# Kernel optimization log

Measured on AMD Instinct MI355X. Metric: run time of the kernel, lower is better.

Reference implementation:

```python
import jax, jax.numpy as jnp
import numpy as np

HEADS = 8
CH = 256
DH = CH // HEADS  # 32
NB = 128          # nb_features
EPS = 1e-4


def setup_inputs() -> dict:
    key = jax.random.key(0)
    ks = jax.random.split(key, 8)
    b, c, h, w = 4, CH, 96, 96
    s = 1.0 / np.sqrt(CH)  # typical linear init scale
    x = jax.random.normal(ks[0], (b, c, h, w), dtype=jnp.float32)
    wq = jax.random.normal(ks[1], (CH, CH), dtype=jnp.float32) * s
    wk = jax.random.normal(ks[2], (CH, CH), dtype=jnp.float32) * s
    wv = jax.random.normal(ks[3], (CH, CH), dtype=jnp.float32) * s
    wo = jax.random.normal(ks[4], (CH, CH), dtype=jnp.float32) * s
    bo = jnp.zeros((CH,), dtype=jnp.float32)
    # FAVOR+ gaussian orthogonal random projection (nb_features, dim_head)
    pm = np.random.default_rng(0)
    blocks = []
    for _ in range(NB // DH):
        qmat, _ = np.linalg.qr(pm.standard_normal((DH, DH)))
        blocks.append(qmat.T)
    proj = np.concatenate(blocks, axis=0)
    # scale rows to chi-distributed norms (scaling=0 default in performer_pytorch)
    norms = np.linalg.norm(pm.standard_normal((NB, DH)), axis=1, keepdims=True)
    proj_mat = jnp.asarray(proj * norms, dtype=jnp.float32)
    wp = jax.random.normal(ks[5], (CH, CH, 1, 1), dtype=jnp.float32) * s
    bp = jnp.zeros((CH,), dtype=jnp.float32)
    return {"x": x, "wq": wq, "wk": wk, "wv": wv, "wo": wo, "bo": bo,
            "proj_mat": proj_mat, "wp": wp, "bp": bp}


def softmax_kernel(data, proj, is_query):
    # data: (b, h, n, d); proj: (m, d). Performer FAVOR+ positive softmax features.
    data_normalizer = data.shape[-1] ** -0.25
    ratio = proj.shape[0] ** -0.5
    data_dash = jnp.einsum('bhnd,md->bhnm', data * data_normalizer, proj)
    diag = (jnp.sum(data * data, axis=-1) * 0.5 * (data_normalizer ** 2))[..., None]
    if is_query:
        m = jnp.max(data_dash, axis=-1, keepdims=True)
    else:
        m = jnp.max(data_dash, axis=(-1, -2), keepdims=True)
    return ratio * (jnp.exp(data_dash - diag - m) + EPS)


def reference(x, wq, wk, wv, wo, bo, proj_mat, wp, bp):
    b, c, h, w = x.shape
    n = h * w
    xf = x.reshape(b, c, n).transpose(0, 2, 1)  # (b, n, c)

    def split_heads(t):
        return t.reshape(b, n, HEADS, DH).transpose(0, 2, 1, 3)  # (b, h, n, d)

    q = split_heads(xf @ wq.T)
    k = split_heads(xf @ wk.T)
    v = split_heads(xf @ wv.T)

    qp = softmax_kernel(q, proj_mat, True)   # (b, h, n, m)
    kp = softmax_kernel(k, proj_mat, False)  # (b, h, n, m)

    # non-causal linear attention
    k_sum = jnp.sum(kp, axis=-2)                                   # (b, h, m)
    d_inv = 1.0 / jnp.einsum('bhnm,bhm->bhn', qp, k_sum)           # (b, h, n)
    ctx = jnp.einsum('bhnm,bhnd->bhmd', kp, v)                     # (b, h, m, d)
    out = jnp.einsum('bhnm,bhmd->bhnd', qp, ctx) * d_inv[..., None]

    out = out.transpose(0, 2, 1, 3).reshape(b, n, c)  # merge heads
    out = out @ wo.T + bo                              # to_out (attn_out_bias=True)
    out = out.transpose(0, 2, 1).reshape(b, c, h, w)
    # 1x1 conv projection
    out = jnp.einsum('bchw,oc->bohw', out, wp[:, :, 0, 0]) + bp[None, :, None, None]
    return out
```

## Files before the change

kernel.cpp:

```cpp
#include <hip/hip_runtime.h>

#define NTOT 9216
#define NORMC 0.42044820762685725f
#define RATIO 0.08838834764831845f
#define FEPS 1e-4f

typedef _Float16 h8 __attribute__((ext_vector_type(8)));
typedef _Float16 h4 __attribute__((ext_vector_type(4)));
typedef float f4 __attribute__((ext_vector_type(4)));

__device__ __forceinline__ void gld16(const _Float16* g, _Float16* l) {
  __builtin_amdgcn_global_load_lds((const __attribute__((address_space(1))) void*)g,
                                   (__attribute__((address_space(3))) void*)l, 16, 0, 0);
}

__global__ __launch_bounds__(256) void prep(
    const float* __restrict__ x, const float* __restrict__ wq,
    const float* __restrict__ wk, const float* __restrict__ wv,
    const float* __restrict__ proj, const float* __restrict__ wo,
    const float* __restrict__ bo, const float* __restrict__ wp,
    const float* __restrict__ bp, _Float16* __restrict__ xT,
    _Float16* __restrict__ Wall, _Float16* __restrict__ projh,
    _Float16* __restrict__ Wc, float* __restrict__ bc) {
  __shared__ float T_s[64][65];
  int r = blockIdx.x, t = threadIdx.x;
  if (r < 2304) {
    int nx = r % 144, rem = r / 144;
    int cy = rem & 3, b = rem >> 2;
    int n0 = nx * 64, c0 = cy * 64;
    for (int i = 0; i < 4; ++i) {
      int f = t + i * 256;
      int cc = f >> 4, n4 = f & 15;
      float4 a = *(const float4*)(x + ((size_t)(b * 256 + c0 + cc)) * NTOT + n0 + n4 * 4);
      T_s[cc][n4 * 4 + 0] = a.x;
      T_s[cc][n4 * 4 + 1] = a.y;
      T_s[cc][n4 * 4 + 2] = a.z;
      T_s[cc][n4 * 4 + 3] = a.w;
    }
    __syncthreads();
    for (int i = 0; i < 2; ++i) {
      int f = t + i * 256;
      int nn = f >> 3, c8 = f & 7;
      h8 hv;
      for (int j = 0; j < 8; ++j) hv[j] = (_Float16)T_s[c8 * 8 + j][nn];
      *(h8*)(xT + ((size_t)(b * NTOT + n0 + nn)) * 256 + c0 + c8 * 8) = hv;
    }
    return;
  }
  int r2 = r - 2304;
  if (r2 < 768) {
    const float* src = (r2 < 256) ? wq + (size_t)r2 * 256
                     : (r2 < 512) ? wk + (size_t)(r2 - 256) * 256
                                  : wv + (size_t)(r2 - 512) * 256;
    Wall[(size_t)r2 * 256 + t] = (_Float16)src[t];
  } else if (r2 < 784) {
    int idx = (r2 - 768) * 256 + t;
    projh[idx] = (_Float16)proj[idx];
  } else {
    int o = r2 - 784;
    float acc = 0.f;
    for (int c = 0; c < 256; ++c) acc += wp[o * 256 + c] * wo[c * 256 + t];
    Wc[o * 256 + t] = (_Float16)acc;
    if (t == 0) {
      float ab = bp[o];
      for (int c = 0; c < 256; ++c) ab += wp[o * 256 + c] * bo[c];
      bc[o] = ab;
    }
  }
}

__global__ __launch_bounds__(256) void qkv_mfma(
    const _Float16* __restrict__ xT, const _Float16* __restrict__ Wall,
    const _Float16* __restrict__ projh, _Float16* __restrict__ q,
    _Float16* __restrict__ k, _Float16* __restrict__ vT,
    float* __restrict__ kmaxp) {
  __shared__ __align__(16) _Float16 A_s[128 * 32];
  __shared__ __align__(16) _Float16 B_s[128 * 32];
  __shared__ __align__(16) _Float16 ktile[64 * 132];
  int bx = blockIdx.x, co0 = blockIdx.y * 128, sel = blockIdx.z;
  int b = bx / 72, ntile = bx % 72;
  int n0 = bx * 128;
  const _Float16* Wb = Wall + (size_t)sel * 65536;
  int t = threadIdx.x, wave = t >> 6, lane = t & 63;
  int lm = lane & 15, lg = lane >> 4;
  int wm = (wave & 1) * 64, wn = (wave >> 1) * 64;
  int srow = wave * 32 + (lane >> 2);
  int scol = ((lane & 3) ^ ((lane >> 3) & 3)) * 8;
  const _Float16* gA = Wb + (size_t)(co0 + srow) * 256 + scol;
  const _Float16* gB = xT + (size_t)(n0 + srow) * 256 + scol;
  _Float16* lA = A_s + wave * 1024;
  _Float16* lB = B_s + wave * 1024;
  int pg = (lg ^ ((lm >> 1) & 3)) * 8;
  f4 acc[4][4] = {};
  if (sel < 2) {
    for (int kt = 0; kt < 8; ++kt) {
      int c0 = kt * 32;
      __syncthreads();
      gld16(gA + c0, lA);
      gld16(gA + c0 + 16 * 256, lA + 512);
      gld16(gB + c0, lB);
      gld16(gB + c0 + 16 * 256, lB + 512);
      __syncthreads();
      h8 a[4], bf[4];
#pragma unroll
      for (int mi = 0; mi < 4; ++mi) a[mi] = *(const h8*)&A_s[(wm + mi * 16 + lm) * 32 + pg];
#pragma unroll
      for (int ni = 0; ni < 4; ++ni) bf[ni] = *(const h8*)&B_s[(wn + ni * 16 + lm) * 32 + pg];
#pragma unroll
      for (int mi = 0; mi < 4; ++mi)
#pragma unroll
        for (int ni = 0; ni < 4; ++ni)
          acc[mi][ni] = __builtin_amdgcn_mfma_f32_16x16x32_f16(a[mi], bf[ni], acc[mi][ni], 0, 0, 0);
    }
    _Float16* Out = (sel == 0) ? q : k;
#pragma unroll
    for (int mi = 0; mi < 4; ++mi)
#pragma unroll
      for (int ni = 0; ni < 4; ++ni) {
        h4 hv;
#pragma unroll
        for (int r = 0; r < 4; ++r) hv[r] = (_Float16)acc[mi][ni][r];
        *(h4*)(Out + (size_t)(n0 + wn + ni * 16 + lm) * 256 + co0 + wm + mi * 16 + lg * 4) = hv;
      }
    if (sel == 1) {
      h8 pr[8];
#pragma unroll
      for (int mt = 0; mt < 8; ++mt)
        pr[mt] = *(const h8*)&projh[(mt * 16 + lm) * 32 + lg * 8];
      float vmax = -1e30f;
      for (int half = 0; half < 2; ++half) {
        __syncthreads();
        if ((wave >> 1) == half) {
#pragma unroll
          for (int mi = 0; mi < 4; ++mi)
#pragma unroll
            for (int ni = 0; ni < 4; ++ni) {
              h4 hv;
#pragma unroll
              for (int r = 0; r < 4; ++r) hv[r] = (_Float16)acc[mi][ni][r];
              *(h4*)&ktile[(ni * 16 + lm) * 132 + wm + mi * 16 + lg * 4] = hv;
            }
        }
        __syncthreads();
#pragma unroll
        for (int nt2 = 0; nt2 < 4; ++nt2) {
          h8 a = *(const h8*)&ktile[(nt2 * 16 + lm) * 132 + wave * 32 + lg * 8];
#pragma unroll
          for (int mt = 0; mt < 8; ++mt) {
            f4 z = {0.f, 0.f, 0.f, 0.f};
            f4 d = __builtin_amdgcn_mfma_f32_16x16x32_f16(a, pr[mt], z, 0, 0, 0);
            vmax = fmaxf(vmax, fmaxf(fmaxf(d[0], d[1]), fmaxf(d[2], d[3])));
          }
        }
      }
      for (int i = 1; i < 64; i <<= 1) vmax = fmaxf(vmax, __shfl_xor(vmax, i, 64));
      if (lane == 0) {
        int h = (co0 >> 5) + wave;
        kmaxp[(size_t)(b * 8 + h) * 72 + ntile] = NORMC * vmax;
      }
    }
  } else {
    for (int kt = 0; kt < 8; ++kt) {
      int c0 = kt * 32;
      __syncthreads();
      gld16(gA + c0, lA);
      gld16(gA + c0 + 16 * 256, lA + 512);
      gld16(gB + c0, lB);
      gld16(gB + c0 + 16 * 256, lB + 512);
      __syncthreads();
      h8 a[4], bf[4];
#pragma unroll
      for (int mi = 0; mi < 4; ++mi) a[mi] = *(const h8*)&A_s[(wm + mi * 16 + lm) * 32 + pg];
#pragma unroll
      for (int ni = 0; ni < 4; ++ni) bf[ni] = *(const h8*)&B_s[(wn + ni * 16 + lm) * 32 + pg];
#pragma unroll
      for (int mi = 0; mi < 4; ++mi)
#pragma unroll
        for (int ni = 0; ni < 4; ++ni)
          acc[mi][ni] = __builtin_amdgcn_mfma_f32_16x16x32_f16(bf[ni], a[mi], acc[mi][ni], 0, 0, 0);
    }
#pragma unroll
    for (int mi = 0; mi < 4; ++mi)
#pragma unroll
      for (int ni = 0; ni < 4; ++ni) {
        h4 hv;
#pragma unroll
        for (int r = 0; r < 4; ++r) hv[r] = (_Float16)acc[mi][ni][r];
        *(h4*)(vT + ((size_t)(b * 256 + co0 + wm + mi * 16 + lm)) * NTOT +
               ntile * 128 + wn + ni * 16 + lg * 4) = hv;
      }
  }
}

__global__ __launch_bounds__(256) void ctx_mfma(
    const _Float16* __restrict__ k, const _Float16* __restrict__ vT,
    const _Float16* __restrict__ projh, const float* __restrict__ kmaxp,
    float* __restrict__ part) {
  __shared__ __align__(16) _Float16 k_s[128 * 32];
  __shared__ __align__(16) _Float16 vT_s[32 * 136];
  __shared__ __align__(16) _Float16 kpT[128 * 136];
  __shared__ float diag_s[128];
  __shared__ float kmax_sh;
  int bh = blockIdx.y, b = bh >> 3, h = bh & 7;
  int nbase = blockIdx.x * 384;
  int t = threadIdx.x, wave = t >> 6, lane = t & 63, lm = lane & 15, lg = lane >> 4;
  h8 pr[8];
#pragma unroll
  for (int mt = 0; mt < 8; ++mt) pr[mt] = *(const h8*)&projh[(mt * 16 + lm) * 32 + lg * 8];
  {
    float* kred = (float*)kpT;
    if (t < 72) kred[t] = kmaxp[(size_t)bh * 72 + t];
    __syncthreads();
    if (t == 0) {
      float mx = -1e30f;
      for (int i = 0; i < 72; ++i) mx = fmaxf(mx, kred[i]);
      kmax_sh = mx;
    }
    __syncthreads();
  }
  float kmax = kmax_sh;
  int scol = ((lane & 3) ^ ((lane >> 3) & 3)) * 8;
  const _Float16* gK =
      k + ((size_t)(b * NTOT + nbase + wave * 32 + (lane >> 2))) * 256 + h * 32 + scol;
  const _Float16* gV = vT + ((size_t)(b * 256 + h * 32 + (t >> 3))) * NTOT + nbase;
  _Float16* lK = k_s + wave * 1024;
  int pg = (lg ^ ((lm >> 1) & 3)) * 8;
  f4 cacc[2][2] = {};
  float ks[8] = {};
  for (int ch = 0; ch < 3; ++ch) {
    gld16(gK + (size_t)(ch * 128) * 256, lK);
    gld16(gK + (size_t)(ch * 128) * 256 + 16 * 256, lK + 512);
    {
      int d = t >> 3, g = t & 7;
#pragma unroll
      for (int i = 0; i < 2; ++i)
        *(h8*)&vT_s[d * 136 + (i * 8 + g) * 8] = *(const h8*)(gV + ch * 128 + (i * 8 + g) * 8);
    }
    __syncthreads();
    if (t < 128) {
      float s = 0.f;
#pragma unroll
      for (int c = 0; c < 4; ++c) {
        h8 kv = *(const h8*)&k_s[t * 32 + c * 8];
#pragma unroll
        for (int j = 0; j < 8; ++j) s += (float)kv[j] * (float)kv[j];
      }
      diag_s[t] = s * (0.5f * NORMC * NORMC);
    }
    f4 dsh[2][8];
#pragma unroll
    for (int nt = 0; nt < 2; ++nt) {
      h8 a = *(const h8*)&k_s[(wave * 32 + nt * 16 + lm) * 32 + pg];
#pragma unroll
      for (int mt = 0; mt < 8; ++mt) {
        f4 z = {0.f, 0.f, 0.f, 0.f};
        dsh[nt][mt] = __builtin_amdgcn_mfma_f32_16x16x32_f16(a, pr[mt], z, 0, 0, 0);
      }
    }
    __syncthreads();
#pragma unroll
    for (int nt = 0; nt < 2; ++nt)
#pragma unroll
      for (int mt = 0; mt < 8; ++mt) {
        h4 hv;
        float lsum = 0.f;
#pragma unroll
        for (int r = 0; r < 4; ++r) {
          int nl = wave * 32 + nt * 16 + lg * 4 + r;
          float val = RATIO * (__expf(NORMC * dsh[nt][mt][r] - diag_s[nl] - kmax) + FEPS);
          hv[r] = (_Float16)val;
          lsum += val;
        }
        ks[mt] += lsum;
        *(h4*)&kpT[(mt * 16 + lm) * 136 + wave * 32 + nt * 16 + lg * 4] = hv;
      }
    __syncthreads();
#pragma unroll
    for (int k2 = 0; k2 < 4; ++k2) {
      h8 a2[2], b2[2];
#pragma unroll
      for (int mt2 = 0; mt2 < 2; ++mt2)
        a2[mt2] = *(const h8*)&kpT[(wave * 32 + mt2 * 16 + lm) * 136 + k2 * 32 + lg * 8];
#pragma unroll
      for (int dt = 0; dt < 2; ++dt)
        b2[dt] = *(const h8*)&vT_s[(dt * 16 + lm) * 136 + k2 * 32 + lg * 8];
#pragma unroll
      for (int mt2 = 0; mt2 < 2; ++mt2)
#pragma unroll
        for (int dt = 0; dt < 2; ++dt)
          cacc[mt2][dt] =
              __builtin_amdgcn_mfma_f32_16x16x32_f16(a2[mt2], b2[dt], cacc[mt2][dt], 0, 0, 0);
    }
    __syncthreads();
  }
  float* pp = part + (size_t)(blockIdx.y * 24 + blockIdx.x) * 4224;
#pragma unroll
  for (int mt2 = 0; mt2 < 2; ++mt2)
#pragma unroll
    for (int dt = 0; dt < 2; ++dt)
      *(f4*)(pp + (dt * 16 + lm) * 128 + wave * 32 + mt2 * 16 + lg * 4) = cacc[mt2][dt];
  float* redk = (float*)kpT;
#pragma unroll
  for (int mt = 0; mt < 8; ++mt) {
    float s = ks[mt];
    s += __shfl_xor(s, 16, 64);
    s += __shfl_xor(s, 32, 64);
    if (lg == 0) redk[wave * 128 + mt * 16 + lm] = s;
  }
  __syncthreads();
  if (t < 128)
    pp[32 * 128 + t] = redk[t] + redk[128 + t] + redk[256 + t] + redk[384 + t];
}

__global__ __launch_bounds__(256) void reduce_ctx(
    const float* __restrict__ part, _Float16* __restrict__ ctxT_g,
    float* __restrict__ ksum_g) {
  int bh = blockIdx.x >> 2, qtr = blockIdx.x & 3;
  int t = threadIdx.x;
  const float* pb = part + (size_t)bh * 24 * 4224;
  for (int it = 0; it < 5; ++it) {
    int lc = it * 256 + t;
    if (lc < 1056) {
      int cell = qtr * 1056 + lc;
      float s = 0.f;
      for (int p = 0; p < 24; ++p) s += pb[(size_t)p * 4224 + cell];
      int d = cell >> 7, m = cell & 127;
      if (d < 32) ctxT_g[(size_t)bh * 4096 + d * 128 + m] = (_Float16)s;
      else ksum_g[(size_t)bh * 128 + m] = s;
    }
  }
}

__global__ __launch_bounds__(256) void attn_mfma(
    const _Float16* __restrict__ q, const _Float16* __restrict__ projh,
    const _Float16* __restrict__ ctxT_g, const float* __restrict__ ksum_g,
    _Float16* __restrict__ attn) {
  __shared__ __align__(16) _Float16 q_sh[128 * 32];
  __shared__ __align__(16) _Float16 qp_s[128 * 136];
  __shared__ float ksum_s[128];
  int n0 = blockIdx.x * 128;
  int bh = blockIdx.y, b = bh >> 3, h = bh & 7;
  int t = threadIdx.x, wave = t >> 6, lane = t & 63, lm = lane & 15, lg = lane >> 4;
  h8 pr[8];
#pragma unroll
  for (int mt = 0; mt < 8; ++mt) pr[mt] = *(const h8*)&projh[(mt * 16 + lm) * 32 + lg * 8];
  int scol = ((lane & 3) ^ ((lane >> 3) & 3)) * 8;
  const _Float16* gQ =
      q + ((size_t)(b * NTOT + n0 + wave * 32 + (lane >> 2))) * 256 + h * 32 + scol;
  gld16(gQ, q_sh + wave * 1024);
  gld16(gQ + 16 * 256, q_sh + wave * 1024 + 512);
  h8 ac[2][4];
#pragma unroll
  for (int dt = 0; dt < 2; ++dt)
#pragma unroll
    for (int k2 = 0; k2 < 4; ++k2)
      ac[dt][k2] = *(const h8*)&ctxT_g[(size_t)bh * 4096 + (dt * 16 + lm) * 128 + k2 * 32 + lg * 8];
  if (t < 128) ksum_s[t] = ksum_g[(size_t)bh * 128 + t];
  __syncthreads();
  int pg = (lg ^ ((lm >> 1) & 3)) * 8;
  float diag_r[2];
#pragma unroll
  for (int nt = 0; nt < 2; ++nt) {
    int n = wave * 32 + nt * 16 + lm;
    float s = 0.f;
#pragma unroll
    for (int c = 0; c < 4; ++c) {
      h8 qv = *(const h8*)&q_sh[n * 32 + c * 8];
#pragma unroll
      for (int j = 0; j < 8; ++j) s += (float)qv[j] * (float)qv[j];
    }
    diag_r[nt] = s * (0.5f * NORMC * NORMC);
  }
  f4 dsh[2][8];
#pragma unroll
  for (int nt = 0; nt < 2; ++nt) {
    h8 qf = *(const h8*)&q_sh[(wave * 32 + nt * 16 + lm) * 32 + pg];
#pragma unroll
    for (int mt = 0; mt < 8; ++mt) {
      f4 z = {0.f, 0.f, 0.f, 0.f};
      dsh[nt][mt] = __builtin_amdgcn_mfma_f32_16x16x32_f16(pr[mt], qf, z, 0, 0, 0);
    }
  }
  float den_r[2];
#pragma unroll
  for (int nt = 0; nt < 2; ++nt) {
    float mx = -1e30f;
#pragma unroll
    for (int mt = 0; mt < 8; ++mt)
#pragma unroll
      for (int r = 0; r < 4; ++r) mx = fmaxf(mx, dsh[nt][mt][r]);
    mx = fmaxf(mx, __shfl_xor(mx, 16, 64));
    mx = fmaxf(mx, __shfl_xor(mx, 32, 64));
    float den = 0.f;
#pragma unroll
    for (int mt = 0; mt < 8; ++mt) {
      h4 hv;
#pragma unroll
      for (int r = 0; r < 4; ++r) {
        float val = RATIO * (__expf(NORMC * (dsh[nt][mt][r] - mx) - diag_r[nt]) + FEPS);
        hv[r] = (_Float16)val;
        den += val * ksum_s[mt * 16 + lg * 4 + r];
      }
      *(h4*)&qp_s[(wave * 32 + nt * 16 + lm) * 136 + mt * 16 + lg * 4] = hv;
    }
    den += __shfl_xor(den, 16, 64);
    den += __shfl_xor(den, 32, 64);
    den_r[nt] = 1.f / den;
  }
  __syncthreads();
  f4 oacc[2][2] = {};
#pragma unroll
  for (int k2 = 0; k2 < 4; ++k2) {
    h8 bq[2];
#pragma unroll
    for (int nt = 0; nt < 2; ++nt)
      bq[nt] = *(const h8*)&qp_s[(wave * 32 + nt * 16 + lm) * 136 + k2 * 32 + lg * 8];
#pragma unroll
    for (int dt = 0; dt < 2; ++dt)
#pragma unroll
      for (int nt = 0; nt < 2; ++nt)
        oacc[dt][nt] = __builtin_amdgcn_mfma_f32_16x16x32_f16(ac[dt][k2], bq[nt], oacc[dt][nt], 0, 0, 0);
  }
#pragma unroll
  for (int dt = 0; dt < 2; ++dt)
#pragma unroll
    for (int nt = 0; nt < 2; ++nt) {
      int n = wave * 32 + nt * 16 + lm;
      h4 hv;
#pragma unroll
      for (int r = 0; r < 4; ++r) hv[r] = (_Float16)(oacc[dt][nt][r] * den_r[nt]);
      *(h4*)(attn + ((size_t)(b * NTOT + n0 + n)) * 256 + h * 32 + dt * 16 + lg * 4) = hv;
    }
}

__global__ __launch_bounds__(256) void out_mfma(
    const _Float16* __restrict__ Wc, const _Float16* __restrict__ attn,
    const float* __restrict__ bc, float* __restrict__ out) {
  __shared__ __align__(16) _Float16 A_s[128 * 32];
  __shared__ __align__(16) _Float16 B_s[128 * 32];
  int bx = blockIdx.x;
  int o0 = blockIdx.y * 128;
  int b = bx / 72, nb0 = (bx % 72) * 128;
  int t = threadIdx.x, wave = t >> 6, lane = t & 63;
  int lm = lane & 15, lg = lane >> 4;
  int wm = (wave & 1) * 64, wn = (wave >> 1) * 64;
  int srow = wave * 32 + (lane >> 2);
  int scol = ((lane & 3) ^ ((lane >> 3) & 3)) * 8;
  const _Float16* gA = Wc + (size_t)(o0 + srow) * 256 + scol;
  const _Float16* gB = attn + (size_t)(b * NTOT + nb0 + srow) * 256 + scol;
  _Float16* lA = A_s + wave * 1024;
  _Float16* lB = B_s + wave * 1024;
  int pg = (lg ^ ((lm >> 1) & 3)) * 8;
  f4 acc[4][4] = {};
  for (int kt = 0; kt < 8; ++kt) {
    int c0 = kt * 32;
    __syncthreads();
    gld16(gA + c0, lA);
    gld16(gA + c0 + 16 * 256, lA + 512);
    gld16(gB + c0, lB);
    gld16(gB + c0 + 16 * 256, lB + 512);
    __syncthreads();
    h8 a[4], bf[4];
#pragma unroll
    for (int mi = 0; mi < 4; ++mi) a[mi] = *(const h8*)&A_s[(wm + mi * 16 + lm) * 32 + pg];
#pragma unroll
    for (int ni = 0; ni < 4; ++ni) bf[ni] = *(const h8*)&B_s[(wn + ni * 16 + lm) * 32 + pg];
#pragma unroll
    for (int mi = 0; mi < 4; ++mi)
#pragma unroll
      for (int ni = 0; ni < 4; ++ni)
        acc[mi][ni] = __builtin_amdgcn_mfma_f32_16x16x32_f16(bf[ni], a[mi], acc[mi][ni], 0, 0, 0);
  }
#pragma unroll
  for (int mi = 0; mi < 4; ++mi) {
    int o = o0 + wm + mi * 16 + lm;
    float bias = bc[o];
#pragma unroll
    for (int ni = 0; ni < 4; ++ni) {
      f4 ov = acc[mi][ni];
      float4 st = make_float4(ov[0] + bias, ov[1] + bias, ov[2] + bias, ov[3] + bias);
      *(float4*)(out + ((size_t)(b * 256 + o)) * NTOT + nb0 + wn + ni * 16 + lg * 4) = st;
    }
  }
}

extern "C" void kernel_launch(void* const* d_in, const int* in_sizes, int n_in,
                              void* d_out, int out_size, void* d_ws, size_t ws_size,
                              hipStream_t stream) {
  const float* x = (const float*)d_in[0];
  const float* wq = (const float*)d_in[1];
  const float* wk = (const float*)d_in[2];
  const float* wv = (const float*)d_in[3];
  const float* wo = (const float*)d_in[4];
  const float* bo = (const float*)d_in[5];
  const float* proj = (const float*)d_in[6];
  const float* wp = (const float*)d_in[7];
  const float* bp = (const float*)d_in[8];
  float* out = (float*)d_out;
  float* ws = (float*)d_ws;

  float* part = ws;
  float* kmaxp = part + 3244032;
  float* ksum_g = kmaxp + 2304;
  float* bc = ksum_g + 4096;
  _Float16* hb = (_Float16*)(bc + 256);
  const size_t THALF = (size_t)4 * NTOT * 256;
  _Float16* q_h = hb;
  _Float16* k_h = q_h + THALF;
  _Float16* xT = k_h + THALF;
  _Float16* vTg = xT + THALF;
  _Float16* Wall = vTg + THALF;
  _Float16* Wc = Wall + 768 * 256;
  _Float16* projh = Wc + 65536;
  _Float16* ctxT_g = projh + 4096;

  prep<<<3344, 256, 0, stream>>>(x, wq, wk, wv, proj, wo, bo, wp, bp,
                                 xT, Wall, projh, Wc, bc);
  qkv_mfma<<<dim3(288, 2, 3), 256, 0, stream>>>(xT, Wall, projh, q_h, k_h, vTg, kmaxp);
  ctx_mfma<<<dim3(24, 32), 256, 0, stream>>>(k_h, vTg, projh, kmaxp, part);
  reduce_ctx<<<128, 256, 0, stream>>>(part, ctxT_g, ksum_g);
  attn_mfma<<<dim3(72, 32), 256, 0, stream>>>(q_h, projh, ctxT_g, ksum_g, xT);
  out_mfma<<<dim3(288, 2), 256, 0, stream>>>(Wc, xT, bc, out);
}
```

Before: 216.6 us.

## Double-buffer LDS tiles in GEMM kernels and prefetch K chunks in ctx

The qkv and out GEMM kernels now keep two LDS stages in a shared pool. The next K-slice's global-to-LDS loads are issued before the MFMAs on the current slice, and each iteration has one barrier instead of two. The two separate q/k and v loop copies in qkv are merged into one loop with a select on MFMA operand order. In ctx_mfma the first K tile load is issued before the kmax reduction, and later tiles are prefetched after the barrier, so load latency overlaps with compute. LDS use grows in the GEMMs (32KB, with ktile aliased onto the pool), which may lower occupancy. The correctness of async-load ordering depends on the single barrier per iteration.

```diff
diff --git a/kernel.cpp b/kernel.cpp
--- a/kernel.cpp
+++ b/kernel.cpp
@@ -74,9 +74,7 @@
     const _Float16* __restrict__ projh, _Float16* __restrict__ q,
     _Float16* __restrict__ k, _Float16* __restrict__ vT,
     float* __restrict__ kmaxp) {
-  __shared__ __align__(16) _Float16 A_s[128 * 32];
-  __shared__ __align__(16) _Float16 B_s[128 * 32];
-  __shared__ __align__(16) _Float16 ktile[64 * 132];
+  __shared__ __align__(16) _Float16 pool[16384];
   int bx = blockIdx.x, co0 = blockIdx.y * 128, sel = blockIdx.z;
   int b = bx / 72, ntile = bx % 72;
   int n0 = bx * 128;
@@ -88,30 +86,48 @@
   int scol = ((lane & 3) ^ ((lane >> 3) & 3)) * 8;
   const _Float16* gA = Wb + (size_t)(co0 + srow) * 256 + scol;
   const _Float16* gB = xT + (size_t)(n0 + srow) * 256 + scol;
-  _Float16* lA = A_s + wave * 1024;
-  _Float16* lB = B_s + wave * 1024;
+  int so = wave * 1024;
   int pg = (lg ^ ((lm >> 1) & 3)) * 8;
   f4 acc[4][4] = {};
-  if (sel < 2) {
-    for (int kt = 0; kt < 8; ++kt) {
-      int c0 = kt * 32;
-      __syncthreads();
-      gld16(gA + c0, lA);
-      gld16(gA + c0 + 16 * 256, lA + 512);
-      gld16(gB + c0, lB);
-      gld16(gB + c0 + 16 * 256, lB + 512);
-      __syncthreads();
-      h8 a[4], bf[4];
-#pragma unroll
-      for (int mi = 0; mi < 4; ++mi) a[mi] = *(const h8*)&A_s[(wm + mi * 16 + lm) * 32 + pg];
-#pragma unroll
-      for (int ni = 0; ni < 4; ++ni) bf[ni] = *(const h8*)&B_s[(wn + ni * 16 + lm) * 32 + pg];
+  gld16(gA, pool + so);
+  gld16(gA + 16 * 256, pool + so + 512);
+  gld16(gB, pool + 8192 + so);
+  gld16(gB + 16 * 256, pool + 8192 + so + 512);
+  __syncthreads();
+#pragma unroll
+  for (int kt = 0; kt < 8; ++kt) {
+    int cur = (kt & 1) << 12;
+    int nxt = cur ^ 4096;
+    if (kt < 7) {
+      int c0 = (kt + 1) * 32;
+      gld16(gA + c0, pool + nxt + so);
+      gld16(gA + c0 + 16 * 256, pool + nxt + so + 512);
+      gld16(gB + c0, pool + 8192 + nxt + so);
+      gld16(gB + c0 + 16 * 256, pool + 8192 + nxt + so + 512);
+    }
+    h8 a[4], bf[4];
+#pragma unroll
+    for (int mi = 0; mi < 4; ++mi)
+      a[mi] = *(const h8*)&pool[cur + (wm + mi * 16 + lm) * 32 + pg];
+#pragma unroll
+    for (int ni = 0; ni < 4; ++ni)
+      bf[ni] = *(const h8*)&pool[8192 + cur + (wn + ni * 16 + lm) * 32 + pg];
+    if (sel < 2) {
 #pragma unroll
       for (int mi = 0; mi < 4; ++mi)
 #pragma unroll
         for (int ni = 0; ni < 4; ++ni)
           acc[mi][ni] = __builtin_amdgcn_mfma_f32_16x16x32_f16(a[mi], bf[ni], acc[mi][ni], 0, 0, 0);
-    }
+    } else {
+#pragma unroll
+      for (int mi = 0; mi < 4; ++mi)
+#pragma unroll
+        for (int ni = 0; ni < 4; ++ni)
+          acc[mi][ni] = __builtin_amdgcn_mfma_f32_16x16x32_f16(bf[ni], a[mi], acc[mi][ni], 0, 0, 0);
+    }
+    __syncthreads();
+  }
+  if (sel < 2) {
     _Float16* Out = (sel == 0) ? q : k;
 #pragma unroll
     for (int mi = 0; mi < 4; ++mi)
@@ -123,6 +139,7 @@
         *(h4*)(Out + (size_t)(n0 + wn + ni * 16 + lm) * 256 + co0 + wm + mi * 16 + lg * 4) = hv;
       }
     if (sel == 1) {
+      _Float16* ktile = pool;
       h8 pr[8];
 #pragma unroll
       for (int mt = 0; mt < 8; ++mt)
@@ -160,25 +177,6 @@
       }
     }
   } else {
-    for (int kt = 0; kt < 8; ++kt) {
-      int c0 = kt * 32;
-      __syncthreads();
-      gld16(gA + c0, lA);
-      gld16(gA + c0 + 16 * 256, lA + 512);
-      gld16(gB + c0, lB);
-      gld16(gB + c0 + 16 * 256, lB + 512);
-      __syncthreads();
-      h8 a[4], bf[4];
-#pragma unroll
-      for (int mi = 0; mi < 4; ++mi) a[mi] = *(const h8*)&A_s[(wm + mi * 16 + lm) * 32 + pg];
-#pragma unroll
-      for (int ni = 0; ni < 4; ++ni) bf[ni] = *(const h8*)&B_s[(wn + ni * 16 + lm) * 32 + pg];
-#pragma unroll
-      for (int mi = 0; mi < 4; ++mi)
-#pragma unroll
-        for (int ni = 0; ni < 4; ++ni)
-          acc[mi][ni] = __builtin_amdgcn_mfma_f32_16x16x32_f16(bf[ni], a[mi], acc[mi][ni], 0, 0, 0);
-    }
 #pragma unroll
     for (int mi = 0; mi < 4; ++mi)
 #pragma unroll
@@ -207,29 +205,29 @@
   h8 pr[8];
 #pragma unroll
   for (int mt = 0; mt < 8; ++mt) pr[mt] = *(const h8*)&projh[(mt * 16 + lm) * 32 + lg * 8];
-  {
-    float* kred = (float*)kpT;
-    if (t < 72) kred[t] = kmaxp[(size_t)bh * 72 + t];
-    __syncthreads();
-    if (t == 0) {
-      float mx = -1e30f;
-      for (int i = 0; i < 72; ++i) mx = fmaxf(mx, kred[i]);
-      kmax_sh = mx;
-    }
-    __syncthreads();
-  }
-  float kmax = kmax_sh;
   int scol = ((lane & 3) ^ ((lane >> 3) & 3)) * 8;
   const _Float16* gK =
       k + ((size_t)(b * NTOT + nbase + wave * 32 + (lane >> 2))) * 256 + h * 32 + scol;
   const _Float16* gV = vT + ((size_t)(b * 256 + h * 32 + (t >> 3))) * NTOT + nbase;
   _Float16* lK = k_s + wave * 1024;
+  gld16(gK, lK);
+  gld16(gK + 16 * 256, lK + 512);
+  {
+    float* kred = (float*)kpT;
+    if (t < 72) kred[t] = kmaxp[(size_t)bh * 72 + t];
+    __syncthreads();
+    if (t == 0) {
+      float mx = -1e30f;
+      for (int i = 0; i < 72; ++i) mx = fmaxf(mx, kred[i]);
+      kmax_sh = mx;
+    }
+    __syncthreads();
+  }
+  float kmax = kmax_sh;
   int pg = (lg ^ ((lm >> 1) & 3)) * 8;
   f4 cacc[2][2] = {};
   float ks[8] = {};
   for (int ch = 0; ch < 3; ++ch) {
-    gld16(gK + (size_t)(ch * 128) * 256, lK);
-    gld16(gK + (size_t)(ch * 128) * 256 + 16 * 256, lK + 512);
     {
       int d = t >> 3, g = t & 7;
 #pragma unroll
@@ -258,6 +256,10 @@
       }
     }
     __syncthreads();
+    if (ch < 2) {
+      gld16(gK + (size_t)((ch + 1) * 128) * 256, lK);
+      gld16(gK + (size_t)((ch + 1) * 128) * 256 + 16 * 256, lK + 512);
+    }
 #pragma unroll
     for (int nt = 0; nt < 2; ++nt)
 #pragma unroll
@@ -436,8 +438,7 @@
 __global__ __launch_bounds__(256) void out_mfma(
     const _Float16* __restrict__ Wc, const _Float16* __restrict__ attn,
     const float* __restrict__ bc, float* __restrict__ out) {
-  __shared__ __align__(16) _Float16 A_s[128 * 32];
-  __shared__ __align__(16) _Float16 B_s[128 * 32];
+  __shared__ __align__(16) _Float16 pool[16384];
   int bx = blockIdx.x;
   int o0 = blockIdx.y * 128;
   int b = bx / 72, nb0 = (bx % 72) * 128;
@@ -448,28 +449,38 @@
   int scol = ((lane & 3) ^ ((lane >> 3) & 3)) * 8;
   const _Float16* gA = Wc + (size_t)(o0 + srow) * 256 + scol;
   const _Float16* gB = attn + (size_t)(b * NTOT + nb0 + srow) * 256 + scol;
-  _Float16* lA = A_s + wave * 1024;
-  _Float16* lB = B_s + wave * 1024;
+  int so = wave * 1024;
   int pg = (lg ^ ((lm >> 1) & 3)) * 8;
   f4 acc[4][4] = {};
+  gld16(gA, pool + so);
+  gld16(gA + 16 * 256, pool + so + 512);
+  gld16(gB, pool + 8192 + so);
+  gld16(gB + 16 * 256, pool + 8192 + so + 512);
+  __syncthreads();
+#pragma unroll
   for (int kt = 0; kt < 8; ++kt) {
-    int c0 = kt * 32;
-    __syncthreads();
-    gld16(gA + c0, lA);
-    gld16(gA + c0 + 16 * 256, lA + 512);
-    gld16(gB + c0, lB);
-    gld16(gB + c0 + 16 * 256, lB + 512);
-    __syncthreads();
+    int cur = (kt & 1) << 12;
+    int nxt = cur ^ 4096;
+    if (kt < 7) {
+      int c0 = (kt + 1) * 32;
+      gld16(gA + c0, pool + nxt + so);
+      gld16(gA + c0 + 16 * 256, pool + nxt + so + 512);
+      gld16(gB + c0, pool + 8192 + nxt + so);
+      gld16(gB + c0 + 16 * 256, pool + 8192 + nxt + so + 512);
+    }
     h8 a[4], bf[4];
 #pragma unroll
-    for (int mi = 0; mi < 4; ++mi) a[mi] = *(const h8*)&A_s[(wm + mi * 16 + lm) * 32 + pg];
-#pragma unroll
-    for (int ni = 0; ni < 4; ++ni) bf[ni] = *(const h8*)&B_s[(wn + ni * 16 + lm) * 32 + pg];
+    for (int mi = 0; mi < 4; ++mi)
+      a[mi] = *(const h8*)&pool[cur + (wm + mi * 16 + lm) * 32 + pg];
+#pragma unroll
+    for (int ni = 0; ni < 4; ++ni)
+      bf[ni] = *(const h8*)&pool[8192 + cur + (wn + ni * 16 + lm) * 32 + pg];
 #pragma unroll
     for (int mi = 0; mi < 4; ++mi)
 #pragma unroll
       for (int ni = 0; ni < 4; ++ni)
         acc[mi][ni] = __builtin_amdgcn_mfma_f32_16x16x32_f16(bf[ni], a[mi], acc[mi][ni], 0, 0, 0);
+    __syncthreads();
   }
 #pragma unroll
   for (int mi = 0; mi < 4; ++mi) {
```

After: 219.7 us. No clear change (+1.5%).

## Remap blocks to XCDs for L2 locality and software-pipeline ctx/out loads

Applied to the files above, without the earlier changes.

Flattens the grids of qkv, ctx, attn and out kernels and remaps block IDs so that blocks sharing the same input tile or (batch, head) land on the same XCD, improving L2 reuse. ctx_mfma prefetches the next chunk of K (via global_load_lds) and V (into registers) during the current chunk's compute. out_mfma uses double-buffered LDS with partial vmcnt waits in place of full syncthreads. These changes add manual waitcnt and barrier handling, which risks ordering bugs, and the double buffer uses more LDS.

```diff
diff --git a/kernel.cpp b/kernel.cpp
--- a/kernel.cpp
+++ b/kernel.cpp
@@ -77,7 +77,12 @@
   __shared__ __align__(16) _Float16 A_s[128 * 32];
   __shared__ __align__(16) _Float16 B_s[128 * 32];
   __shared__ __align__(16) _Float16 ktile[64 * 132];
-  int bx = blockIdx.x, co0 = blockIdx.y * 128, sel = blockIdx.z;
+  int id = blockIdx.x;
+  int xcd = id & 7, slot = id >> 3;
+  int bx = xcd * 36 + slot / 6;
+  int variant = slot % 6;
+  int sel = variant % 3;
+  int co0 = (variant / 3) * 128;
   int b = bx / 72, ntile = bx % 72;
   int n0 = bx * 128;
   const _Float16* Wb = Wall + (size_t)sel * 65536;
@@ -201,12 +206,27 @@
   __shared__ __align__(16) _Float16 kpT[128 * 136];
   __shared__ float diag_s[128];
   __shared__ float kmax_sh;
-  int bh = blockIdx.y, b = bh >> 3, h = bh & 7;
-  int nbase = blockIdx.x * 384;
+  int id = blockIdx.x;
+  int xcd = id & 7, slot = id >> 3;
+  int grp = xcd * 12 + slot / 8;
+  int h = slot % 8;
+  int nx = grp % 24, b = grp / 24;
+  int bh = b * 8 + h;
+  int nbase = nx * 384;
   int t = threadIdx.x, wave = t >> 6, lane = t & 63, lm = lane & 15, lg = lane >> 4;
   h8 pr[8];
 #pragma unroll
   for (int mt = 0; mt < 8; ++mt) pr[mt] = *(const h8*)&projh[(mt * 16 + lm) * 32 + lg * 8];
+  int scol = ((lane & 3) ^ ((lane >> 3) & 3)) * 8;
+  const _Float16* gK =
+      k + ((size_t)(b * NTOT + nbase + wave * 32 + (lane >> 2))) * 256 + h * 32 + scol;
+  const _Float16* gV = vT + ((size_t)(b * 256 + h * 32 + (t >> 3))) * NTOT + nbase;
+  _Float16* lK = k_s + wave * 1024;
+  int vd = t >> 3, vg = t & 7;
+  gld16(gK, lK);
+  gld16(gK + 16 * 256, lK + 512);
+  h8 vr0 = *(const h8*)(gV + vg * 8);
+  h8 vr1 = *(const h8*)(gV + 64 + vg * 8);
   {
     float* kred = (float*)kpT;
     if (t < 72) kred[t] = kmaxp[(size_t)bh * 72 + t];
@@ -219,24 +239,16 @@
     __syncthreads();
   }
   float kmax = kmax_sh;
-  int scol = ((lane & 3) ^ ((lane >> 3) & 3)) * 8;
-  const _Float16* gK =
-      k + ((size_t)(b * NTOT + nbase + wave * 32 + (lane >> 2))) * 256 + h * 32 + scol;
-  const _Float16* gV = vT + ((size_t)(b * 256 + h * 32 + (t >> 3))) * NTOT + nbase;
-  _Float16* lK = k_s + wave * 1024;
   int pg = (lg ^ ((lm >> 1) & 3)) * 8;
   f4 cacc[2][2] = {};
   float ks[8] = {};
+#pragma unroll 1
   for (int ch = 0; ch < 3; ++ch) {
-    gld16(gK + (size_t)(ch * 128) * 256, lK);
-    gld16(gK + (size_t)(ch * 128) * 256 + 16 * 256, lK + 512);
-    {
-      int d = t >> 3, g = t & 7;
-#pragma unroll
-      for (int i = 0; i < 2; ++i)
-        *(h8*)&vT_s[d * 136 + (i * 8 + g) * 8] = *(const h8*)(gV + ch * 128 + (i * 8 + g) * 8);
-    }
-    __syncthreads();
+    *(h8*)&vT_s[vd * 136 + vg * 8] = vr0;
+    *(h8*)&vT_s[vd * 136 + 64 + vg * 8] = vr1;
+    asm volatile("s_waitcnt vmcnt(0) lgkmcnt(0)" ::: "memory");
+    __builtin_amdgcn_s_barrier();
+    __builtin_amdgcn_sched_barrier(0);
     if (t < 128) {
       float s = 0.f;
 #pragma unroll
@@ -257,7 +269,15 @@
         dsh[nt][mt] = __builtin_amdgcn_mfma_f32_16x16x32_f16(a, pr[mt], z, 0, 0, 0);
       }
     }
-    __syncthreads();
+    asm volatile("s_waitcnt lgkmcnt(0)" ::: "memory");
+    __builtin_amdgcn_s_barrier();
+    __builtin_amdgcn_sched_barrier(0);
+    if (ch < 2) {
+      gld16(gK + (size_t)((ch + 1) * 128) * 256, lK);
+      gld16(gK + (size_t)((ch + 1) * 128) * 256 + 16 * 256, lK + 512);
+      vr0 = *(const h8*)(gV + (ch + 1) * 128 + vg * 8);
+      vr1 = *(const h8*)(gV + (ch + 1) * 128 + 64 + vg * 8);
+    }
 #pragma unroll
     for (int nt = 0; nt < 2; ++nt)
 #pragma unroll
@@ -274,7 +294,9 @@
         ks[mt] += lsum;
         *(h4*)&kpT[(mt * 16 + lm) * 136 + wave * 32 + nt * 16 + lg * 4] = hv;
       }
-    __syncthreads();
+    asm volatile("s_waitcnt lgkmcnt(0)" ::: "memory");
+    __builtin_amdgcn_s_barrier();
+    __builtin_amdgcn_sched_barrier(0);
 #pragma unroll
     for (int k2 = 0; k2 < 4; ++k2) {
       h8 a2[2], b2[2];
@@ -291,9 +313,9 @@
           cacc[mt2][dt] =
               __builtin_amdgcn_mfma_f32_16x16x32_f16(a2[mt2], b2[dt], cacc[mt2][dt], 0, 0, 0);
     }
-    __syncthreads();
-  }
-  float* pp = part + (size_t)(blockIdx.y * 24 + blockIdx.x) * 4224;
+    __builtin_amdgcn_s_barrier();
+  }
+  float* pp = part + (size_t)(bh * 24 + nx) * 4224;
 #pragma unroll
   for (int mt2 = 0; mt2 < 2; ++mt2)
 #pragma unroll
@@ -338,8 +360,13 @@
   __shared__ __align__(16) _Float16 q_sh[128 * 32];
   __shared__ __align__(16) _Float16 qp_s[128 * 136];
   __shared__ float ksum_s[128];
-  int n0 = blockIdx.x * 128;
-  int bh = blockIdx.y, b = bh >> 3, h = bh & 7;
+  int id = blockIdx.x;
+  int xcd = id & 7, slot = id >> 3;
+  int grp = xcd * 36 + slot / 8;
+  int h = slot % 8;
+  int nb = grp % 72, b = grp / 72;
+  int bh = b * 8 + h;
+  int n0 = nb * 128;
   int t = threadIdx.x, wave = t >> 6, lane = t & 63, lm = lane & 15, lg = lane >> 4;
   h8 pr[8];
 #pragma unroll
@@ -436,11 +463,12 @@
 __global__ __launch_bounds__(256) void out_mfma(
     const _Float16* __restrict__ Wc, const _Float16* __restrict__ attn,
     const float* __restrict__ bc, float* __restrict__ out) {
-  __shared__ __align__(16) _Float16 A_s[128 * 32];
-  __shared__ __align__(16) _Float16 B_s[128 * 32];
-  int bx = blockIdx.x;
-  int o0 = blockIdx.y * 128;
-  int b = bx / 72, nb0 = (bx % 72) * 128;
+  __shared__ __align__(16) _Float16 pool[16384];
+  int id = blockIdx.x;
+  int xcd = id & 7, slot = id >> 3;
+  int tile = xcd * 36 + slot / 2;
+  int o0 = (slot & 1) * 128;
+  int b = tile / 72, nb0 = (tile % 72) * 128;
   int t = threadIdx.x, wave = t >> 6, lane = t & 63;
   int lm = lane & 15, lg = lane >> 4;
   int wm = (wave & 1) * 64, wn = (wave >> 1) * 64;
@@ -448,28 +476,42 @@
   int scol = ((lane & 3) ^ ((lane >> 3) & 3)) * 8;
   const _Float16* gA = Wc + (size_t)(o0 + srow) * 256 + scol;
   const _Float16* gB = attn + (size_t)(b * NTOT + nb0 + srow) * 256 + scol;
-  _Float16* lA = A_s + wave * 1024;
-  _Float16* lB = B_s + wave * 1024;
+  int so = wave * 1024;
   int pg = (lg ^ ((lm >> 1) & 3)) * 8;
   f4 acc[4][4] = {};
+  gld16(gA, pool + so);
+  gld16(gA + 16 * 256, pool + so + 512);
+  gld16(gB, pool + 8192 + so);
+  gld16(gB + 16 * 256, pool + 8192 + so + 512);
+#pragma unroll 1
   for (int kt = 0; kt < 8; ++kt) {
-    int c0 = kt * 32;
-    __syncthreads();
-    gld16(gA + c0, lA);
-    gld16(gA + c0 + 16 * 256, lA + 512);
-    gld16(gB + c0, lB);
-    gld16(gB + c0 + 16 * 256, lB + 512);
-    __syncthreads();
+    int cur = (kt & 1) << 12;
+    int nxt = cur ^ 4096;
+    if (kt < 7) {
+      int c0 = (kt + 1) * 32;
+      gld16(gA + c0, pool + nxt + so);
+      gld16(gA + c0 + 16 * 256, pool + nxt + so + 512);
+      gld16(gB + c0, pool + 8192 + nxt + so);
+      gld16(gB + c0 + 16 * 256, pool + 8192 + nxt + so + 512);
+      asm volatile("s_waitcnt vmcnt(4)" ::: "memory");
+    } else {
+      asm volatile("s_waitcnt vmcnt(0)" ::: "memory");
+    }
+    __builtin_amdgcn_s_barrier();
+    __builtin_amdgcn_sched_barrier(0);
     h8 a[4], bf[4];
 #pragma unroll
-    for (int mi = 0; mi < 4; ++mi) a[mi] = *(const h8*)&A_s[(wm + mi * 16 + lm) * 32 + pg];
-#pragma unroll
-    for (int ni = 0; ni < 4; ++ni) bf[ni] = *(const h8*)&B_s[(wn + ni * 16 + lm) * 32 + pg];
+    for (int mi = 0; mi < 4; ++mi)
+      a[mi] = *(const h8*)&pool[cur + (wm + mi * 16 + lm) * 32 + pg];
+#pragma unroll
+    for (int ni = 0; ni < 4; ++ni)
+      bf[ni] = *(const h8*)&pool[8192 + cur + (wn + ni * 16 + lm) * 32 + pg];
 #pragma unroll
     for (int mi = 0; mi < 4; ++mi)
 #pragma unroll
       for (int ni = 0; ni < 4; ++ni)
         acc[mi][ni] = __builtin_amdgcn_mfma_f32_16x16x32_f16(bf[ni], a[mi], acc[mi][ni], 0, 0, 0);
+    __builtin_amdgcn_s_barrier();
   }
 #pragma unroll
   for (int mi = 0; mi < 4; ++mi) {
@@ -516,9 +558,9 @@
 
   prep<<<3344, 256, 0, stream>>>(x, wq, wk, wv, proj, wo, bo, wp, bp,
                                  xT, Wall, projh, Wc, bc);
-  qkv_mfma<<<dim3(288, 2, 3), 256, 0, stream>>>(xT, Wall, projh, q_h, k_h, vTg, kmaxp);
-  ctx_mfma<<<dim3(24, 32), 256, 0, stream>>>(k_h, vTg, projh, kmaxp, part);
+  qkv_mfma<<<1728, 256, 0, stream>>>(xT, Wall, projh, q_h, k_h, vTg, kmaxp);
+  ctx_mfma<<<768, 256, 0, stream>>>(k_h, vTg, projh, kmaxp, part);
   reduce_ctx<<<128, 256, 0, stream>>>(part, ctxT_g, ksum_g);
-  attn_mfma<<<dim3(72, 32), 256, 0, stream>>>(q_h, projh, ctxT_g, ksum_g, xT);
-  out_mfma<<<dim3(288, 2), 256, 0, stream>>>(Wc, xT, bc, out);
-}
+  attn_mfma<<<2304, 256, 0, stream>>>(q_h, projh, ctxT_g, ksum_g, xT);
+  out_mfma<<<576, 256, 0, stream>>>(Wc, xT, bc, out);
+}
```

After: 220.3 us. Within noise of the previous version (+1.7%).

## Prefetch next K/V chunk in ctx kernel, alias shared buffers, widen reduce grid

Applied to the files above, without the earlier changes.

In ctx_mfma the next chunk's K tile (async global-to-LDS) and V rows (into registers) are now loaded while the exp/feature stage runs, and syncthreads are replaced with explicit waitcnt plus s_barrier. This hides global load latency behind compute. qkv_mfma and attn_mfma alias their shared buffers into one pool to cut LDS use and raise occupancy, which needs an added barrier in attn_mfma. reduce_ctx is reshaped into 1056 small blocks, one output row each, to spread the reduction across more CUs.

```diff
diff --git a/kernel.cpp b/kernel.cpp
--- a/kernel.cpp
+++ b/kernel.cpp
@@ -74,9 +74,10 @@
     const _Float16* __restrict__ projh, _Float16* __restrict__ q,
     _Float16* __restrict__ k, _Float16* __restrict__ vT,
     float* __restrict__ kmaxp) {
-  __shared__ __align__(16) _Float16 A_s[128 * 32];
-  __shared__ __align__(16) _Float16 B_s[128 * 32];
-  __shared__ __align__(16) _Float16 ktile[64 * 132];
+  __shared__ __align__(16) _Float16 pool[8448];
+  _Float16* A_s = pool;
+  _Float16* B_s = pool + 4096;
+  _Float16* ktile = pool;
   int bx = blockIdx.x, co0 = blockIdx.y * 128, sel = blockIdx.z;
   int b = bx / 72, ntile = bx % 72;
   int n0 = bx * 128;
@@ -207,6 +208,16 @@
   h8 pr[8];
 #pragma unroll
   for (int mt = 0; mt < 8; ++mt) pr[mt] = *(const h8*)&projh[(mt * 16 + lm) * 32 + lg * 8];
+  int scol = ((lane & 3) ^ ((lane >> 3) & 3)) * 8;
+  const _Float16* gK =
+      k + ((size_t)(b * NTOT + nbase + wave * 32 + (lane >> 2))) * 256 + h * 32 + scol;
+  const _Float16* gV = vT + ((size_t)(b * 256 + h * 32 + (t >> 3))) * NTOT + nbase;
+  _Float16* lK = k_s + wave * 1024;
+  int vd = t >> 3, vg = t & 7;
+  gld16(gK, lK);
+  gld16(gK + 16 * 256, lK + 512);
+  h8 vr0 = *(const h8*)(gV + vg * 8);
+  h8 vr1 = *(const h8*)(gV + 64 + vg * 8);
   {
     float* kred = (float*)kpT;
     if (t < 72) kred[t] = kmaxp[(size_t)bh * 72 + t];
@@ -219,24 +230,16 @@
     __syncthreads();
   }
   float kmax = kmax_sh;
-  int scol = ((lane & 3) ^ ((lane >> 3) & 3)) * 8;
-  const _Float16* gK =
-      k + ((size_t)(b * NTOT + nbase + wave * 32 + (lane >> 2))) * 256 + h * 32 + scol;
-  const _Float16* gV = vT + ((size_t)(b * 256 + h * 32 + (t >> 3))) * NTOT + nbase;
-  _Float16* lK = k_s + wave * 1024;
   int pg = (lg ^ ((lm >> 1) & 3)) * 8;
   f4 cacc[2][2] = {};
   float ks[8] = {};
+#pragma unroll 1
   for (int ch = 0; ch < 3; ++ch) {
-    gld16(gK + (size_t)(ch * 128) * 256, lK);
-    gld16(gK + (size_t)(ch * 128) * 256 + 16 * 256, lK + 512);
-    {
-      int d = t >> 3, g = t & 7;
-#pragma unroll
-      for (int i = 0; i < 2; ++i)
-        *(h8*)&vT_s[d * 136 + (i * 8 + g) * 8] = *(const h8*)(gV + ch * 128 + (i * 8 + g) * 8);
-    }
-    __syncthreads();
+    *(h8*)&vT_s[vd * 136 + vg * 8] = vr0;
+    *(h8*)&vT_s[vd * 136 + 64 + vg * 8] = vr1;
+    asm volatile("s_waitcnt vmcnt(0) lgkmcnt(0)" ::: "memory");
+    __builtin_amdgcn_s_barrier();
+    __builtin_amdgcn_sched_barrier(0);
     if (t < 128) {
       float s = 0.f;
 #pragma unroll
@@ -257,7 +260,15 @@
         dsh[nt][mt] = __builtin_amdgcn_mfma_f32_16x16x32_f16(a, pr[mt], z, 0, 0, 0);
       }
     }
-    __syncthreads();
+    asm volatile("s_waitcnt lgkmcnt(0)" ::: "memory");
+    __builtin_amdgcn_s_barrier();
+    __builtin_amdgcn_sched_barrier(0);
+    if (ch < 2) {
+      gld16(gK + (size_t)((ch + 1) * 128) * 256, lK);
+      gld16(gK + (size_t)((ch + 1) * 128) * 256 + 16 * 256, lK + 512);
+      vr0 = *(const h8*)(gV + (ch + 1) * 128 + vg * 8);
+      vr1 = *(const h8*)(gV + (ch + 1) * 128 + 64 + vg * 8);
+    }
 #pragma unroll
     for (int nt = 0; nt < 2; ++nt)
 #pragma unroll
@@ -274,7 +285,9 @@
         ks[mt] += lsum;
         *(h4*)&kpT[(mt * 16 + lm) * 136 + wave * 32 + nt * 16 + lg * 4] = hv;
       }
-    __syncthreads();
+    asm volatile("s_waitcnt lgkmcnt(0)" ::: "memory");
+    __builtin_amdgcn_s_barrier();
+    __builtin_amdgcn_sched_barrier(0);
 #pragma unroll
     for (int k2 = 0; k2 < 4; ++k2) {
       h8 a2[2], b2[2];
@@ -291,7 +304,7 @@
           cacc[mt2][dt] =
               __builtin_amdgcn_mfma_f32_16x16x32_f16(a2[mt2], b2[dt], cacc[mt2][dt], 0, 0, 0);
     }
-    __syncthreads();
+    __builtin_amdgcn_s_barrier();
   }
   float* pp = part + (size_t)(blockIdx.y * 24 + blockIdx.x) * 4224;
 #pragma unroll
@@ -312,32 +325,27 @@
     pp[32 * 128 + t] = redk[t] + redk[128 + t] + redk[256 + t] + redk[384 + t];
 }
 
-__global__ __launch_bounds__(256) void reduce_ctx(
+__global__ __launch_bounds__(128) void reduce_ctx(
     const float* __restrict__ part, _Float16* __restrict__ ctxT_g,
     float* __restrict__ ksum_g) {
-  int bh = blockIdx.x >> 2, qtr = blockIdx.x & 3;
+  int bh = blockIdx.x / 33, row = blockIdx.x % 33;
   int t = threadIdx.x;
-  const float* pb = part + (size_t)bh * 24 * 4224;
-  for (int it = 0; it < 5; ++it) {
-    int lc = it * 256 + t;
-    if (lc < 1056) {
-      int cell = qtr * 1056 + lc;
-      float s = 0.f;
-      for (int p = 0; p < 24; ++p) s += pb[(size_t)p * 4224 + cell];
-      int d = cell >> 7, m = cell & 127;
-      if (d < 32) ctxT_g[(size_t)bh * 4096 + d * 128 + m] = (_Float16)s;
-      else ksum_g[(size_t)bh * 128 + m] = s;
-    }
-  }
+  const float* pb = part + (size_t)bh * 24 * 4224 + row * 128 + t;
+  float s = 0.f;
+#pragma unroll
+  for (int p = 0; p < 24; ++p) s += pb[(size_t)p * 4224];
+  if (row < 32) ctxT_g[(size_t)bh * 4096 + row * 128 + t] = (_Float16)s;
+  else ksum_g[(size_t)bh * 128 + t] = s;
 }
 
 __global__ __launch_bounds__(256) void attn_mfma(
     const _Float16* __restrict__ q, const _Float16* __restrict__ projh,
     const _Float16* __restrict__ ctxT_g, const float* __restrict__ ksum_g,
     _Float16* __restrict__ attn) {
-  __shared__ __align__(16) _Float16 q_sh[128 * 32];
-  __shared__ __align__(16) _Float16 qp_s[128 * 136];
+  __shared__ __align__(16) _Float16 apool[128 * 136];
   __shared__ float ksum_s[128];
+  _Float16* q_sh = apool;
+  _Float16* qp_s = apool;
   int n0 = blockIdx.x * 128;
   int bh = blockIdx.y, b = bh >> 3, h = bh & 7;
   int t = threadIdx.x, wave = t >> 6, lane = t & 63, lm = lane & 15, lg = lane >> 4;
@@ -381,6 +389,7 @@
       dsh[nt][mt] = __builtin_amdgcn_mfma_f32_16x16x32_f16(pr[mt], qf, z, 0, 0, 0);
     }
   }
+  __syncthreads();
   float den_r[2];
 #pragma unroll
   for (int nt = 0; nt < 2; ++nt) {
@@ -518,7 +527,7 @@
                                  xT, Wall, projh, Wc, bc);
   qkv_mfma<<<dim3(288, 2, 3), 256, 0, stream>>>(xT, Wall, projh, q_h, k_h, vTg, kmaxp);
   ctx_mfma<<<dim3(24, 32), 256, 0, stream>>>(k_h, vTg, projh, kmaxp, part);
-  reduce_ctx<<<128, 256, 0, stream>>>(part, ctxT_g, ksum_g);
+  reduce_ctx<<<1056, 128, 0, stream>>>(part, ctxT_g, ksum_g);
   attn_mfma<<<dim3(72, 32), 256, 0, stream>>>(q_h, projh, ctxT_g, ksum_g, xT);
   out_mfma<<<dim3(288, 2), 256, 0, stream>>>(Wc, xT, bc, out);
 }
```

New measurement: 217.3 us. No clear change (+0.4%).
